# Optimization experiments

Hardware: AMD Instinct MI355X
Metric: run time of the kernel (lower is better)

## Reference

```python
import jax, jax.numpy as jnp
import numpy as np

SOFTENING = 1e-6
EPS = 1e-9
CUTOFF = 0.1
K_NEG = 4
MARGIN = 1.0
KE_FACTOR = 1e-3


def setup_inputs() -> dict:
    key = jax.random.key(0)
    ks = jax.random.split(key, 16)
    B, S, D8, W = 4, 2048, 8, 16
    N = B * S
    return {
        "positions_2d": jax.random.normal(ks[0], (B, S, 2), dtype=jnp.float32),
        "masses": jax.random.uniform(ks[1], (B, S, 1), dtype=jnp.float32),
        "vel_2d": jax.random.normal(ks[2], (N, 2), dtype=jnp.float32),
        "pos_8d": jax.random.normal(ks[3], (N, D8), dtype=jnp.float32),
        "pos_pos_2d": jax.random.normal(ks[4], (N, 2), dtype=jnp.float32),
        "pos_pos_8d": jax.random.normal(ks[5], (N, D8), dtype=jnp.float32),
        "positive_masses": jax.random.uniform(ks[6], (N, 1), dtype=jnp.float32),
        "neg_pos_2d": jax.random.normal(ks[7], (N * K_NEG, 2), dtype=jnp.float32),
        "neg_pos_8d": jax.random.normal(ks[8], (N * K_NEG, D8), dtype=jnp.float32),
        "neg_masses": jax.random.uniform(ks[9], (N * K_NEG, 1), dtype=jnp.float32),
        "exp_masses": jax.random.uniform(ks[10], (N * K_NEG, 1), dtype=jnp.float32),
        "G": jnp.float32(1.0),
        "repulsion_strength": jnp.float32(0.5),
        "well_centers": jax.random.normal(ks[11], (W, D8), dtype=jnp.float32),
        "well_strength": jnp.float32(0.1),
        "temperature": jnp.float32(1.0),
        "entropy_coeff": jnp.float32(0.01),
    }


def _calculate_forces(positions_2d, masses, G, repulsion_strength):
    # positions_2d: [B,S,2], masses: [B,S,1]
    B, S, _ = positions_2d.shape
    # diff[b,i,j] = pos[b,j] - pos[b,i]  -> [B,S,S,2]
    diff = positions_2d[:, None, :, :] - positions_2d[:, :, None, :]
    dist_sq = jnp.sum(diff * diff, axis=-1) + SOFTENING  # [B,S,S]
    dist = jnp.sqrt(dist_sq)
    diag = jnp.eye(S, dtype=bool)  # [S,S], broadcasts over B
    dist_safe = jnp.where(diag, 1.0, dist)
    dist_sq_safe = jnp.where(diag, 1.0, dist_sq)
    mm = masses[:, :, None, 0] * masses[:, None, :, 0]  # [B,S,S]
    attractive = jax.nn.relu(G) * mm / dist_sq_safe
    rep_strength = jax.nn.relu(repulsion_strength)
    repulsive = rep_strength * jax.nn.relu(1.0 - dist_safe / CUTOFF) / (dist_sq_safe * dist_safe + EPS)
    total_mag = repulsive - attractive  # [B,S,S]
    force_vectors = total_mag[..., None] * diff / (dist_safe[..., None] + EPS)
    return jnp.sum(force_vectors, axis=2)  # [B,S,2]


def _cdist(a, b):
    # Euclidean cdist: [N,D] x [W,D] -> [N,W]; W=16 so dense is cheap
    d = a[:, None, :] - b[None, :, :]
    return jnp.sqrt(jnp.sum(d * d, axis=-1))


def _grand_unifying_loss(pos_2d, vel_2d, pos_8d, masses_flat, pos_pos_2d, pos_pos_8d,
                         positive_masses, neg_pos_2d, neg_pos_8d, neg_masses, exp_masses,
                         G, well_centers, well_strength, temperature, entropy_coeff):
    Gp = jax.nn.relu(G)
    dist_pos_2d = jnp.linalg.norm(pos_2d - pos_pos_2d, axis=-1) + EPS  # [N]
    pe_pairwise_pos = -Gp * (masses_flat * positive_masses)[:, 0] / dist_pos_2d
    pos_2d_rep = jnp.repeat(pos_2d, K_NEG, axis=0)  # [N*K,2]
    dist_neg_2d = jnp.linalg.norm(pos_2d_rep - neg_pos_2d, axis=-1) + EPS
    pe_pairwise_neg = -Gp * (exp_masses * neg_masses)[:, 0] / dist_neg_2d

    ws = jax.nn.relu(well_strength)
    all_pos_8d = jnp.concatenate([pos_8d, pos_pos_8d], axis=0)  # [2N,8]
    min_dist_pos = jnp.min(_cdist(all_pos_8d, well_centers), axis=1)
    pe_well_pos = ws * min_dist_pos ** 2
    all_neg_8d = jnp.concatenate([jnp.repeat(pos_8d, K_NEG, axis=0), neg_pos_8d], axis=0)
    min_dist_neg = jnp.min(_cdist(all_neg_8d, well_centers), axis=1)
    pe_well_neg = ws * min_dist_neg ** 2

    U_pos = jnp.mean(pe_pairwise_pos) + jnp.mean(pe_well_pos)
    U_neg = jnp.mean(pe_pairwise_neg) + jnp.mean(pe_well_neg)
    batch_variance = jnp.mean(jnp.var(all_pos_8d, axis=0, ddof=1))  # torch.var is unbiased
    entropy_term = jax.nn.relu(temperature) * jax.nn.relu(entropy_coeff) * batch_variance
    F_pos = U_pos - entropy_term
    F_neg = U_neg - entropy_term
    free_energy_loss = jax.nn.relu(MARGIN + F_pos - F_neg)
    # Original: mean(masses[N,1] * ke[N]) broadcasts to an [N,N] outer product;
    # mean of the outer product == mean(m) * mean(ke) (same value and gradients)
    ke = jnp.sum(vel_2d * vel_2d, axis=-1)  # [N]
    ke_loss = KE_FACTOR * 0.5 * jnp.mean(masses_flat) * jnp.mean(ke)
    return free_energy_loss + ke_loss


def reference(positions_2d, masses, vel_2d, pos_8d, pos_pos_2d, pos_pos_8d,
              positive_masses, neg_pos_2d, neg_pos_8d, neg_masses, exp_masses,
              G, repulsion_strength, well_centers, well_strength, temperature, entropy_coeff):
    forces = _calculate_forces(positions_2d, masses, G, repulsion_strength)
    pos_flat = positions_2d.reshape(-1, 2)
    masses_flat = masses.reshape(-1, 1)
    loss = _grand_unifying_loss(pos_flat, vel_2d, pos_8d, masses_flat, pos_pos_2d,
                                pos_pos_8d, positive_masses, neg_pos_2d, neg_pos_8d,
                                neg_masses, exp_masses, G, well_centers, well_strength,
                                temperature, entropy_coeff)
    return forces, loss
```

## Files before the change

### kernel.cpp

```cpp
#include <hip/hip_runtime.h>

#define SEQ    2048
#define N_PTS  8192
#define NK     32768
#define N2     16384
#define NACC   22
#define NLOSSBLK 256
#define NFORCE   1024
#define SLOT_DOUBLES (NLOSSBLK * NACC)
#define CTR_OFFSET   (SLOT_DOUBLES * 8)

__device__ __forceinline__ float frcp(float x)  { return __builtin_amdgcn_rcpf(x); }
__device__ __forceinline__ float fsqrt_(float x){ return __builtin_amdgcn_sqrtf(x); }

__device__ __forceinline__ float min_dist2(float4 a, float4 b, const float* __restrict__ wc)
{
    float best = 3.4e38f;
    #pragma unroll
    for (int w = 0; w < 16; ++w) {
        const float* c = &wc[w * 8];
        float d, s;
        d = a.x - c[0]; s = d * d;
        d = a.y - c[1]; s = fmaf(d, d, s);
        d = a.z - c[2]; s = fmaf(d, d, s);
        d = a.w - c[3]; s = fmaf(d, d, s);
        d = b.x - c[4]; s = fmaf(d, d, s);
        d = b.y - c[5]; s = fmaf(d, d, s);
        d = b.z - c[6]; s = fmaf(d, d, s);
        d = b.w - c[7]; s = fmaf(d, d, s);
        best = fminf(best, s);
    }
    return best;
}


__global__ __launch_bounds__(256, 4) void force_kernel(
    const float* __restrict__ pos,
    const float* __restrict__ mass,
    const float* __restrict__ Gptr,
    const float* __restrict__ Rptr,
    float* __restrict__ out)
{
    __shared__ float4 s4[SEQ];
    __shared__ float  rf[2][4][8];

    const int tid = threadIdx.x;
    const int fb  = blockIdx.x;
    const int b   = fb >> 8;
    const int it  = fb & 255;
    const int rowbase = b * SEQ;

    const float2* p2 = (const float2*)pos;
    for (int k = tid; k < SEQ; k += 256) {
        const float2 v = p2[rowbase + k];
        s4[k] = make_float4(v.x, v.y, mass[rowbase + k], 0.0f);
    }
    const float Gv = fmaxf(Gptr[0], 0.0f);
    const float Rv = fmaxf(Rptr[0], 0.0f);
    __syncthreads();

    const int il = tid & 7;
    const int js = tid >> 3;
    const int iloc = it * 8 + il;
    const float px = s4[iloc].x;
    const float py = s4[iloc].y;
    const float ci = Gv * s4[iloc].z;

    auto pair = [&](const float4 q, float& fx, float& fy) {
        const float dx = q.x - px;
        const float dy = q.y - py;
        const float r2 = fmaf(dx, dx, fmaf(dy, dy, 1e-6f));
        const float r  = fsqrt_(r2);
        const float rp = r + 1e-9f;
        float mor = -(ci * q.z) * frcp(r2 * rp);
        const float t = fmaf(-10.0f, r, 1.0f);
        if (t > 0.0f) {
            mor += (Rv * t) * frcp(fmaf(r2, r, 1e-9f) * rp);
        }
        fx = fmaf(mor, dx, fx);
        fy = fmaf(mor, dy, fy);
    };

    float fx0 = 0.0f, fy0 = 0.0f, fx1 = 0.0f, fy1 = 0.0f;
    float fx2 = 0.0f, fy2 = 0.0f, fx3 = 0.0f, fy3 = 0.0f;
    #pragma unroll 4
    for (int kk = 0; kk < 64; kk += 4) {
        const float4 q0 = s4[js + 32 * (kk + 0)];
        const float4 q1 = s4[js + 32 * (kk + 1)];
        const float4 q2 = s4[js + 32 * (kk + 2)];
        const float4 q3 = s4[js + 32 * (kk + 3)];
        pair(q0, fx0, fy0);
        pair(q1, fx1, fy1);
        pair(q2, fx2, fy2);
        pair(q3, fx3, fy3);
    }
    float vx = (fx0 + fx1) + (fx2 + fx3);
    float vy = (fy0 + fy1) + (fy2 + fy3);

    #pragma unroll
    for (int off = 32; off >= 8; off >>= 1) {
        vx += __shfl_down(vx, off, 64);
        vy += __shfl_down(vy, off, 64);
    }
    const int lane = tid & 63, wid = tid >> 6;
    if (lane < 8) { rf[0][wid][lane] = vx; rf[1][wid][lane] = vy; }
    __syncthreads();
    if (tid < 16) {
        const int comp = tid >> 3, i2 = tid & 7;
        const float s = (rf[comp][0][i2] + rf[comp][1][i2])
                      + (rf[comp][2][i2] + rf[comp][3][i2]);
        out[(rowbase + it * 8 + i2) * 2 + comp] = s;
    }
}

__global__ __launch_bounds__(256) void loss_kernel(
    const float* __restrict__ pos,
    const float* __restrict__ mass,
    const float* __restrict__ vel,
    const float* __restrict__ pos8,
    const float* __restrict__ pp2,
    const float* __restrict__ pp8,
    const float* __restrict__ pmass,
    const float* __restrict__ negp2,
    const float* __restrict__ negp8,
    const float* __restrict__ negm,
    const float* __restrict__ expm,
    const float* __restrict__ Gptr,
    const float* __restrict__ wellc,
    const float* __restrict__ wstr,
    const float* __restrict__ tPtr,
    const float* __restrict__ ecPtr,
    float* __restrict__ out,
    double* __restrict__ slots,
    unsigned int* __restrict__ ctr)
{
    const int tid = threadIdx.x;
    const int blk = blockIdx.x;

    __shared__ float  wc[128];
    __shared__ double red[4][NACC];
    __shared__ int    lastflag;

    if (tid < 128) wc[tid] = wellc[tid];
    if (tid == 0)  lastflag = 0;
    __syncthreads();

    const int lb  = blk;
    const int idx = lb * 256 + tid;

    double acc[NACC];
    #pragma unroll
    for (int k = 0; k < NACC; ++k) acc[k] = 0.0;

    {
        const float* row = (idx < NK) ? (pos8 + (idx >> 2) * 8)
                                      : (negp8 + (idx - NK) * 8);
        const float4 a = ((const float4*)row)[0];
        const float4 b = ((const float4*)row)[1];
        acc[3] = (double)min_dist2(a, b, wc);
    }
    if (idx < NK) {
        const int i = idx >> 2;
        const float dx = pos[i * 2 + 0] - negp2[idx * 2 + 0];
        const float dy = pos[i * 2 + 1] - negp2[idx * 2 + 1];
        const float d  = fsqrt_(fmaf(dx, dx, dy * dy)) + 1e-9f;
        acc[1] = (double)(expm[idx] * negm[idx] / d);
    }
    if (idx < N2) {
        const float* row = (idx < N_PTS) ? (pos8 + idx * 8)
                                         : (pp8 + (idx - N_PTS) * 8);
        const float4 a = ((const float4*)row)[0];
        const float4 b = ((const float4*)row)[1];
        acc[2] = (double)min_dist2(a, b, wc);
        acc[4]  = (double)a.x;  acc[12] = (double)(a.x * a.x);
        acc[5]  = (double)a.y;  acc[13] = (double)(a.y * a.y);
        acc[6]  = (double)a.z;  acc[14] = (double)(a.z * a.z);
        acc[7]  = (double)a.w;  acc[15] = (double)(a.w * a.w);
        acc[8]  = (double)b.x;  acc[16] = (double)(b.x * b.x);
        acc[9]  = (double)b.y;  acc[17] = (double)(b.y * b.y);
        acc[10] = (double)b.z;  acc[18] = (double)(b.z * b.z);
        acc[11] = (double)b.w;  acc[19] = (double)(b.w * b.w);
    }
    if (idx < N_PTS) {
        const float dx = pos[idx * 2 + 0] - pp2[idx * 2 + 0];
        const float dy = pos[idx * 2 + 1] - pp2[idx * 2 + 1];
        const float d  = fsqrt_(fmaf(dx, dx, dy * dy)) + 1e-9f;
        acc[0]  = (double)(mass[idx] * pmass[idx] / d);
        acc[20] = (double)mass[idx];
        const float vx = vel[idx * 2 + 0];
        const float vy = vel[idx * 2 + 1];
        acc[21] = (double)fmaf(vx, vx, vy * vy);
    }

    const int lane = tid & 63, wid = tid >> 6;
    #pragma unroll
    for (int k = 0; k < NACC; ++k) {
        double v = acc[k];
        for (int off = 32; off > 0; off >>= 1) v += __shfl_down(v, off, 64);
        if (lane == 0) red[wid][k] = v;
    }
    __syncthreads();
    if (tid < NACC) {
        slots[lb * NACC + tid] = red[0][tid] + red[1][tid] + red[2][tid] + red[3][tid];
    }
    __syncthreads();
    if (tid == 0) {
        __threadfence();
        const unsigned int ticket = atomicAdd(ctr, 1u);
        if (ticket == (NLOSSBLK - 1u) ||
            ticket == 0xAAAAAAAAu + (NLOSSBLK - 1u)) lastflag = 1;
    }
    __syncthreads();
    if (!lastflag) return;

    __threadfence();
    #pragma unroll
    for (int k = 0; k < NACC; ++k) {
        double v = slots[tid * NACC + k];
        for (int off = 32; off > 0; off >>= 1) v += __shfl_down(v, off, 64);
        if (lane == 0) red[wid][k] = v;
    }
    __syncthreads();
    if (tid == 0) {
        double s[NACC];
        #pragma unroll
        for (int k = 0; k < NACC; ++k)
            s[k] = red[0][k] + red[1][k] + red[2][k] + red[3][k];

        const double Gp  = fmax((double)Gptr[0], 0.0);
        const double wsp = fmax((double)wstr[0], 0.0);
        const double T   = fmax((double)tPtr[0], 0.0);
        const double ec  = fmax((double)ecPtr[0], 0.0);
        const double Nd = 8192.0, NKd = 32768.0, N2d = 16384.0, NK2d = 65536.0;

        const double U_pos = -Gp * s[0] / Nd  + wsp * s[2] / N2d;
        const double U_neg = -Gp * s[1] / NKd + wsp * s[3] / NK2d;

        double var = 0.0;
        for (int d = 0; d < 8; ++d) {
            const double sx_ = s[4 + d], sxx = s[12 + d];
            var += (sxx - sx_ * sx_ / N2d) / (N2d - 1.0);
        }
        var *= 0.125;
        const double ent = T * ec * var;
        const double Fp = U_pos - ent, Fn = U_neg - ent;
        double fel = 1.0 + Fp - Fn;
        if (fel < 0.0) fel = 0.0;
        const double ke_loss = 1e-3 * 0.5 * (s[20] / Nd) * (s[21] / Nd);
        out[16384] = (float)(fel + ke_loss);
    }
}

extern "C" void kernel_launch(void* const* d_in, const int* in_sizes, int n_in,
                              void* d_out, int out_size, void* d_ws, size_t ws_size,
                              hipStream_t stream)
{
    const float* pos   = (const float*)d_in[0];
    const float* mass  = (const float*)d_in[1];
    const float* vel   = (const float*)d_in[2];
    const float* pos8  = (const float*)d_in[3];
    const float* pp2   = (const float*)d_in[4];
    const float* pp8   = (const float*)d_in[5];
    const float* pmass = (const float*)d_in[6];
    const float* negp2 = (const float*)d_in[7];
    const float* negp8 = (const float*)d_in[8];
    const float* negm  = (const float*)d_in[9];
    const float* expm  = (const float*)d_in[10];
    const float* Gp    = (const float*)d_in[11];
    const float* Rp    = (const float*)d_in[12];
    const float* wellc = (const float*)d_in[13];
    const float* wstr  = (const float*)d_in[14];
    const float* temp  = (const float*)d_in[15];
    const float* ecoef = (const float*)d_in[16];

    float*        out   = (float*)d_out;
    double*       slots = (double*)d_ws;
    unsigned int* ctr   = (unsigned int*)((char*)d_ws + CTR_OFFSET);

    loss_kernel<<<NLOSSBLK, 256, 0, stream>>>(pos, mass, vel, pos8, pp2, pp8,
                                              pmass, negp2, negp8, negm, expm,
                                              Gp, wellc, wstr, temp, ecoef,
                                              out, slots, ctr);
    force_kernel<<<NFORCE, 256, 0, stream>>>(pos, mass, Gp, Rp, out);
}
```

Before: 118.7 us.

## Fuse force and loss kernels into one grid, dedupe pos8 well distances

Merges the force and loss kernels into a single launch, with block-index ranges selecting the role, so the two sets of work can overlap on the GPU. The loss part drops from 256 to 192 blocks by reusing the pos_8d well-distance sum for the repeated negative anchors (multiplied by 4) instead of recomputing it per negative. The atomic-ticket last-block reduction is replaced by a separate one-block finalize kernel, which adds a launch but removes the atomic and the fences. The fused kernel keeps the force kernel's launch bounds and shared memory footprint for every block, which could limit occupancy for the loss blocks.

```diff
diff --git a/kernel.cpp b/kernel.cpp
--- a/kernel.cpp
+++ b/kernel.cpp
@@ -4,11 +4,9 @@
 #define N_PTS  8192
 #define NK     32768
 #define N2     16384
-#define NACC   22
-#define NLOSSBLK 256
+#define NACC   23
+#define NLOSSBLK 192
 #define NFORCE   1024
-#define SLOT_DOUBLES (NLOSSBLK * NACC)
-#define CTR_OFFSET   (SLOT_DOUBLES * 8)
 
 __device__ __forceinline__ float frcp(float x)  { return __builtin_amdgcn_rcpf(x); }
 __device__ __forceinline__ float fsqrt_(float x){ return __builtin_amdgcn_sqrtf(x); }
@@ -33,87 +31,7 @@
     return best;
 }
 
-
-__global__ __launch_bounds__(256, 4) void force_kernel(
-    const float* __restrict__ pos,
-    const float* __restrict__ mass,
-    const float* __restrict__ Gptr,
-    const float* __restrict__ Rptr,
-    float* __restrict__ out)
-{
-    __shared__ float4 s4[SEQ];
-    __shared__ float  rf[2][4][8];
-
-    const int tid = threadIdx.x;
-    const int fb  = blockIdx.x;
-    const int b   = fb >> 8;
-    const int it  = fb & 255;
-    const int rowbase = b * SEQ;
-
-    const float2* p2 = (const float2*)pos;
-    for (int k = tid; k < SEQ; k += 256) {
-        const float2 v = p2[rowbase + k];
-        s4[k] = make_float4(v.x, v.y, mass[rowbase + k], 0.0f);
-    }
-    const float Gv = fmaxf(Gptr[0], 0.0f);
-    const float Rv = fmaxf(Rptr[0], 0.0f);
-    __syncthreads();
-
-    const int il = tid & 7;
-    const int js = tid >> 3;
-    const int iloc = it * 8 + il;
-    const float px = s4[iloc].x;
-    const float py = s4[iloc].y;
-    const float ci = Gv * s4[iloc].z;
-
-    auto pair = [&](const float4 q, float& fx, float& fy) {
-        const float dx = q.x - px;
-        const float dy = q.y - py;
-        const float r2 = fmaf(dx, dx, fmaf(dy, dy, 1e-6f));
-        const float r  = fsqrt_(r2);
-        const float rp = r + 1e-9f;
-        float mor = -(ci * q.z) * frcp(r2 * rp);
-        const float t = fmaf(-10.0f, r, 1.0f);
-        if (t > 0.0f) {
-            mor += (Rv * t) * frcp(fmaf(r2, r, 1e-9f) * rp);
-        }
-        fx = fmaf(mor, dx, fx);
-        fy = fmaf(mor, dy, fy);
-    };
-
-    float fx0 = 0.0f, fy0 = 0.0f, fx1 = 0.0f, fy1 = 0.0f;
-    float fx2 = 0.0f, fy2 = 0.0f, fx3 = 0.0f, fy3 = 0.0f;
-    #pragma unroll 4
-    for (int kk = 0; kk < 64; kk += 4) {
-        const float4 q0 = s4[js + 32 * (kk + 0)];
-        const float4 q1 = s4[js + 32 * (kk + 1)];
-        const float4 q2 = s4[js + 32 * (kk + 2)];
-        const float4 q3 = s4[js + 32 * (kk + 3)];
-        pair(q0, fx0, fy0);
-        pair(q1, fx1, fy1);
-        pair(q2, fx2, fy2);
-        pair(q3, fx3, fy3);
-    }
-    float vx = (fx0 + fx1) + (fx2 + fx3);
-    float vy = (fy0 + fy1) + (fy2 + fy3);
-
-    #pragma unroll
-    for (int off = 32; off >= 8; off >>= 1) {
-        vx += __shfl_down(vx, off, 64);
-        vy += __shfl_down(vy, off, 64);
-    }
-    const int lane = tid & 63, wid = tid >> 6;
-    if (lane < 8) { rf[0][wid][lane] = vx; rf[1][wid][lane] = vy; }
-    __syncthreads();
-    if (tid < 16) {
-        const int comp = tid >> 3, i2 = tid & 7;
-        const float s = (rf[comp][0][i2] + rf[comp][1][i2])
-                      + (rf[comp][2][i2] + rf[comp][3][i2]);
-        out[(rowbase + it * 8 + i2) * 2 + comp] = s;
-    }
-}
-
-__global__ __launch_bounds__(256) void loss_kernel(
+__global__ __launch_bounds__(256, 4) void fused_kernel(
     const float* __restrict__ pos,
     const float* __restrict__ mass,
     const float* __restrict__ vel,
@@ -126,70 +44,144 @@
     const float* __restrict__ negm,
     const float* __restrict__ expm,
     const float* __restrict__ Gptr,
+    const float* __restrict__ Rptr,
     const float* __restrict__ wellc,
-    const float* __restrict__ wstr,
-    const float* __restrict__ tPtr,
-    const float* __restrict__ ecPtr,
     float* __restrict__ out,
-    double* __restrict__ slots,
-    unsigned int* __restrict__ ctr)
+    double* __restrict__ slots)
 {
     const int tid = threadIdx.x;
     const int blk = blockIdx.x;
 
+    if (blk >= NLOSSBLK) {
+        __shared__ float4 s4[SEQ];
+        __shared__ float  rf[2][4][8];
+
+        const int fb = blk - NLOSSBLK;
+        const int b  = fb >> 8;
+        const int it = fb & 255;
+        const int rowbase = b * SEQ;
+
+        const float2* p2 = (const float2*)pos;
+        for (int k = tid; k < SEQ; k += 256) {
+            const float2 v = p2[rowbase + k];
+            s4[k] = make_float4(v.x, v.y, mass[rowbase + k], 0.0f);
+        }
+        const float Gv = fmaxf(Gptr[0], 0.0f);
+        const float Rv = fmaxf(Rptr[0], 0.0f);
+        __syncthreads();
+
+        const int il = tid & 7;
+        const int js = tid >> 3;
+        const int iloc = it * 8 + il;
+        const float px = s4[iloc].x;
+        const float py = s4[iloc].y;
+        const float ci = Gv * s4[iloc].z;
+
+        auto pair = [&](const float4 q, float& fx, float& fy) {
+            const float dx = q.x - px;
+            const float dy = q.y - py;
+            const float r2 = fmaf(dx, dx, fmaf(dy, dy, 1e-6f));
+            const float r  = fsqrt_(r2);
+            const float rp = r + 1e-9f;
+            float mor = -(ci * q.z) * frcp(r2 * rp);
+            const float t = fmaf(-10.0f, r, 1.0f);
+            if (t > 0.0f) {
+                mor += (Rv * t) * frcp(fmaf(r2, r, 1e-9f) * rp);
+            }
+            fx = fmaf(mor, dx, fx);
+            fy = fmaf(mor, dy, fy);
+        };
+
+        float fx0 = 0.0f, fy0 = 0.0f, fx1 = 0.0f, fy1 = 0.0f;
+        float fx2 = 0.0f, fy2 = 0.0f, fx3 = 0.0f, fy3 = 0.0f;
+        #pragma unroll 4
+        for (int kk = 0; kk < 64; kk += 4) {
+            const float4 q0 = s4[js + 32 * (kk + 0)];
+            const float4 q1 = s4[js + 32 * (kk + 1)];
+            const float4 q2 = s4[js + 32 * (kk + 2)];
+            const float4 q3 = s4[js + 32 * (kk + 3)];
+            pair(q0, fx0, fy0);
+            pair(q1, fx1, fy1);
+            pair(q2, fx2, fy2);
+            pair(q3, fx3, fy3);
+        }
+        float vx = (fx0 + fx1) + (fx2 + fx3);
+        float vy = (fy0 + fy1) + (fy2 + fy3);
+
+        #pragma unroll
+        for (int off = 32; off >= 8; off >>= 1) {
+            vx += __shfl_down(vx, off, 64);
+            vy += __shfl_down(vy, off, 64);
+        }
+        const int lane = tid & 63, wid = tid >> 6;
+        if (lane < 8) { rf[0][wid][lane] = vx; rf[1][wid][lane] = vy; }
+        __syncthreads();
+        if (tid < 16) {
+            const int comp = tid >> 3, i2 = tid & 7;
+            const float s = (rf[comp][0][i2] + rf[comp][1][i2])
+                          + (rf[comp][2][i2] + rf[comp][3][i2]);
+            out[(rowbase + it * 8 + i2) * 2 + comp] = s;
+        }
+        return;
+    }
+
     __shared__ float  wc[128];
     __shared__ double red[4][NACC];
-    __shared__ int    lastflag;
 
     if (tid < 128) wc[tid] = wellc[tid];
-    if (tid == 0)  lastflag = 0;
     __syncthreads();
 
-    const int lb  = blk;
-    const int idx = lb * 256 + tid;
+    const int idx = blk * 256 + tid;
 
     double acc[NACC];
     #pragma unroll
     for (int k = 0; k < NACC; ++k) acc[k] = 0.0;
 
-    {
-        const float* row = (idx < NK) ? (pos8 + (idx >> 2) * 8)
-                                      : (negp8 + (idx - NK) * 8);
-        const float4 a = ((const float4*)row)[0];
-        const float4 b = ((const float4*)row)[1];
-        acc[3] = (double)min_dist2(a, b, wc);
-    }
-    if (idx < NK) {
-        const int i = idx >> 2;
-        const float dx = pos[i * 2 + 0] - negp2[idx * 2 + 0];
-        const float dy = pos[i * 2 + 1] - negp2[idx * 2 + 1];
-        const float d  = fsqrt_(fmaf(dx, dx, dy * dy)) + 1e-9f;
-        acc[1] = (double)(expm[idx] * negm[idx] / d);
-    }
-    if (idx < N2) {
-        const float* row = (idx < N_PTS) ? (pos8 + idx * 8)
-                                         : (pp8 + (idx - N_PTS) * 8);
-        const float4 a = ((const float4*)row)[0];
-        const float4 b = ((const float4*)row)[1];
-        acc[2] = (double)min_dist2(a, b, wc);
-        acc[4]  = (double)a.x;  acc[12] = (double)(a.x * a.x);
-        acc[5]  = (double)a.y;  acc[13] = (double)(a.y * a.y);
-        acc[6]  = (double)a.z;  acc[14] = (double)(a.z * a.z);
-        acc[7]  = (double)a.w;  acc[15] = (double)(a.w * a.w);
-        acc[8]  = (double)b.x;  acc[16] = (double)(b.x * b.x);
-        acc[9]  = (double)b.y;  acc[17] = (double)(b.y * b.y);
-        acc[10] = (double)b.z;  acc[18] = (double)(b.z * b.z);
-        acc[11] = (double)b.w;  acc[19] = (double)(b.w * b.w);
-    }
     if (idx < N_PTS) {
+        const float4 a = ((const float4*)(pos8 + idx * 8))[0];
+        const float4 b = ((const float4*)(pos8 + idx * 8))[1];
+        acc[2]  = (double)min_dist2(a, b, wc);
+        acc[5]  = (double)a.x;  acc[13] = (double)(a.x * a.x);
+        acc[6]  = (double)a.y;  acc[14] = (double)(a.y * a.y);
+        acc[7]  = (double)a.z;  acc[15] = (double)(a.z * a.z);
+        acc[8]  = (double)a.w;  acc[16] = (double)(a.w * a.w);
+        acc[9]  = (double)b.x;  acc[17] = (double)(b.x * b.x);
+        acc[10] = (double)b.y;  acc[18] = (double)(b.y * b.y);
+        acc[11] = (double)b.z;  acc[19] = (double)(b.z * b.z);
+        acc[12] = (double)b.w;  acc[20] = (double)(b.w * b.w);
+
         const float dx = pos[idx * 2 + 0] - pp2[idx * 2 + 0];
         const float dy = pos[idx * 2 + 1] - pp2[idx * 2 + 1];
         const float d  = fsqrt_(fmaf(dx, dx, dy * dy)) + 1e-9f;
         acc[0]  = (double)(mass[idx] * pmass[idx] / d);
-        acc[20] = (double)mass[idx];
+        acc[21] = (double)mass[idx];
         const float vx = vel[idx * 2 + 0];
         const float vy = vel[idx * 2 + 1];
-        acc[21] = (double)fmaf(vx, vx, vy * vy);
+        acc[22] = (double)fmaf(vx, vx, vy * vy);
+    } else if (idx < N2) {
+        const int r = idx - N_PTS;
+        const float4 a = ((const float4*)(pp8 + r * 8))[0];
+        const float4 b = ((const float4*)(pp8 + r * 8))[1];
+        acc[3]  = (double)min_dist2(a, b, wc);
+        acc[5]  = (double)a.x;  acc[13] = (double)(a.x * a.x);
+        acc[6]  = (double)a.y;  acc[14] = (double)(a.y * a.y);
+        acc[7]  = (double)a.z;  acc[15] = (double)(a.z * a.z);
+        acc[8]  = (double)a.w;  acc[16] = (double)(a.w * a.w);
+        acc[9]  = (double)b.x;  acc[17] = (double)(b.x * b.x);
+        acc[10] = (double)b.y;  acc[18] = (double)(b.y * b.y);
+        acc[11] = (double)b.z;  acc[19] = (double)(b.z * b.z);
+        acc[12] = (double)b.w;  acc[20] = (double)(b.w * b.w);
+    } else {
+        const int k = idx - N2;
+        const float4 a = ((const float4*)(negp8 + k * 8))[0];
+        const float4 b = ((const float4*)(negp8 + k * 8))[1];
+        acc[4] = (double)min_dist2(a, b, wc);
+
+        const int i = k >> 2;
+        const float dx = pos[i * 2 + 0] - negp2[k * 2 + 0];
+        const float dy = pos[i * 2 + 1] - negp2[k * 2 + 1];
+        const float d  = fsqrt_(fmaf(dx, dx, dy * dy)) + 1e-9f;
+        acc[1] = (double)(expm[k] * negm[k] / d);
     }
 
     const int lane = tid & 63, wid = tid >> 6;
@@ -201,22 +193,25 @@
     }
     __syncthreads();
     if (tid < NACC) {
-        slots[lb * NACC + tid] = red[0][tid] + red[1][tid] + red[2][tid] + red[3][tid];
-    }
-    __syncthreads();
-    if (tid == 0) {
-        __threadfence();
-        const unsigned int ticket = atomicAdd(ctr, 1u);
-        if (ticket == (NLOSSBLK - 1u) ||
-            ticket == 0xAAAAAAAAu + (NLOSSBLK - 1u)) lastflag = 1;
-    }
-    __syncthreads();
-    if (!lastflag) return;
-
-    __threadfence();
+        slots[blk * NACC + tid] = red[0][tid] + red[1][tid] + red[2][tid] + red[3][tid];
+    }
+}
+
+__global__ __launch_bounds__(256) void finalize_kernel(
+    const float* __restrict__ Gptr,
+    const float* __restrict__ wstr,
+    const float* __restrict__ tPtr,
+    const float* __restrict__ ecPtr,
+    const double* __restrict__ slots,
+    float* __restrict__ out)
+{
+    __shared__ double red[4][NACC];
+    const int tid = threadIdx.x;
+    const int lane = tid & 63, wid = tid >> 6;
+
     #pragma unroll
     for (int k = 0; k < NACC; ++k) {
-        double v = slots[tid * NACC + k];
+        double v = (tid < NLOSSBLK) ? slots[tid * NACC + k] : 0.0;
         for (int off = 32; off > 0; off >>= 1) v += __shfl_down(v, off, 64);
         if (lane == 0) red[wid][k] = v;
     }
@@ -225,7 +220,7 @@
         double s[NACC];
         #pragma unroll
         for (int k = 0; k < NACC; ++k)
-            s[k] = red[0][k] + red[1][k] + red[2][k] + red[3][k];
+            s[k] = (red[0][k] + red[1][k]) + (red[2][k] + red[3][k]);
 
         const double Gp  = fmax((double)Gptr[0], 0.0);
         const double wsp = fmax((double)wstr[0], 0.0);
@@ -233,12 +228,14 @@
         const double ec  = fmax((double)ecPtr[0], 0.0);
         const double Nd = 8192.0, NKd = 32768.0, N2d = 16384.0, NK2d = 65536.0;
 
-        const double U_pos = -Gp * s[0] / Nd  + wsp * s[2] / N2d;
-        const double U_neg = -Gp * s[1] / NKd + wsp * s[3] / NK2d;
+        const double S_pos8 = s[2], S_pp8 = s[3], S_neg8 = s[4];
+        const double U_pos = -Gp * s[0] / Nd  + wsp * (S_pos8 + S_pp8) / N2d;
+        const double U_neg = -Gp * s[1] / NKd
+                           + wsp * (4.0 * S_pos8 + S_neg8) / NK2d;
 
         double var = 0.0;
         for (int d = 0; d < 8; ++d) {
-            const double sx_ = s[4 + d], sxx = s[12 + d];
+            const double sx_ = s[5 + d], sxx = s[13 + d];
             var += (sxx - sx_ * sx_ / N2d) / (N2d - 1.0);
         }
         var *= 0.125;
@@ -246,7 +243,7 @@
         const double Fp = U_pos - ent, Fn = U_neg - ent;
         double fel = 1.0 + Fp - Fn;
         if (fel < 0.0) fel = 0.0;
-        const double ke_loss = 1e-3 * 0.5 * (s[20] / Nd) * (s[21] / Nd);
+        const double ke_loss = 1e-3 * 0.5 * (s[21] / Nd) * (s[22] / Nd);
         out[16384] = (float)(fel + ke_loss);
     }
 }
@@ -273,13 +270,11 @@
     const float* temp  = (const float*)d_in[15];
     const float* ecoef = (const float*)d_in[16];
 
-    float*        out   = (float*)d_out;
-    double*       slots = (double*)d_ws;
-    unsigned int* ctr   = (unsigned int*)((char*)d_ws + CTR_OFFSET);
-
-    loss_kernel<<<NLOSSBLK, 256, 0, stream>>>(pos, mass, vel, pos8, pp2, pp8,
-                                              pmass, negp2, negp8, negm, expm,
-                                              Gp, wellc, wstr, temp, ecoef,
-                                              out, slots, ctr);
-    force_kernel<<<NFORCE, 256, 0, stream>>>(pos, mass, Gp, Rp, out);
-}
+    float*  out   = (float*)d_out;
+    double* slots = (double*)d_ws;
+
+    fused_kernel<<<NLOSSBLK + NFORCE, 256, 0, stream>>>(
+        pos, mass, vel, pos8, pp2, pp8, pmass, negp2, negp8, negm, expm,
+        Gp, Rp, wellc, out, slots);
+    finalize_kernel<<<1, 256, 0, stream>>>(Gp, wstr, temp, ecoef, slots, out);
+}
```

Measured after the change: 113.2 us. -4.6%, faster.
